# Kernel optimization log

Measured on AMD Instinct MI355X. Metric: run time of the kernel, lower is better.

## Reference

```python
import jax, jax.numpy as jnp
import numpy as np

HID = 1024
PRED_LEN = 96


def lstm_cell(x, h, c, Wih, Whh, bih, bhh):
    # PyTorch LSTMCell: gates ordered i, f, g, o
    gates = x @ Wih.T + h @ Whh.T + bih + bhh
    i, f, g, o = jnp.split(gates, 4, axis=-1)
    c_new = jax.nn.sigmoid(f) * c + jax.nn.sigmoid(i) * jnp.tanh(g)
    h_new = jax.nn.sigmoid(o) * jnp.tanh(c_new)
    return h_new, c_new


def time_enc(idx, embs):
    # sum of 4 embedding lookups -> [..., time_encode_dim]
    return sum(e[idx[..., k]] for k, e in enumerate(embs))


def setup_inputs() -> dict:
    key = jax.random.key(0)
    ks = jax.random.split(key, 32)
    B, T, IN, OUT, H, TE = 256, 128, 7, 7, HID, 3
    d = {}
    d["x"] = jax.random.normal(ks[0], (B, T, IN), jnp.float32)
    d["y"] = jax.random.normal(ks[1], (B, PRED_LEN, OUT), jnp.float32)
    d["x_time_encode"] = jax.random.randint(ks[2], (B, T, 4), 0, 7)
    d["y_time_encode"] = jax.random.randint(ks[3], (B, PRED_LEN, 4), 0, 7)
    sizes = (12, 31, 24, 7)
    for i, n in enumerate(sizes):
        d[f"emb{i}"] = jax.random.normal(ks[4 + i], (n, TE), jnp.float32)
    ins = (IN + TE, H, H)
    s = float(1.0 / np.sqrt(H))
    for l in range(3):
        d[f"Wih{l}"] = jax.random.uniform(ks[8 + 4 * l], (4 * H, ins[l]), jnp.float32, -s, s)
        d[f"Whh{l}"] = jax.random.uniform(ks[9 + 4 * l], (4 * H, H), jnp.float32, -s, s)
        d[f"bih{l}"] = jax.random.uniform(ks[10 + 4 * l], (4 * H,), jnp.float32, -s, s)
        d[f"bhh{l}"] = jax.random.uniform(ks[11 + 4 * l], (4 * H,), jnp.float32, -s, s)
    d["fcW"] = jax.random.uniform(ks[20], (OUT, H), jnp.float32, -s, s)
    d["fcb"] = jax.random.uniform(ks[21], (OUT,), jnp.float32, -s, s)
    return d


def reference(x, y, x_time_encode, y_time_encode, emb0, emb1, emb2, emb3,
              Wih0, Whh0, bih0, bhh0, Wih1, Whh1, bih1, bhh1,
              Wih2, Whh2, bih2, bhh2, fcW, fcb):
    embs = (emb0, emb1, emb2, emb3)
    layers = ((Wih0, Whh0, bih0, bhh0),
              (Wih1, Whh1, bih1, bhh1),
              (Wih2, Whh2, bih2, bhh2))
    B = x.shape[0]
    H = Whh0.shape[1]

    # encode: concat time embedding, run stacked LSTM over time (dropout_rate=0 -> no-op)
    xin = jnp.concatenate([x, time_enc(x_time_encode, embs)], axis=-1)  # [B,T,in+te]
    h0 = tuple(jnp.zeros((B, H), x.dtype) for _ in range(3))

    def run_layers(hs, cs, inp):
        nh, nc = [], []
        for l, (Wih, Whh, bih, bhh) in enumerate(layers):
            h, c = lstm_cell(inp, hs[l], cs[l], Wih, Whh, bih, bhh)
            nh.append(h)
            nc.append(c)
            inp = h
        return tuple(nh), tuple(nc)

    def enc_step(carry, xt):
        hs, cs = carry
        hs, cs = run_layers(hs, cs, xt)
        return (hs, cs), None

    (hs, cs), _ = jax.lax.scan(enc_step, (h0, h0), xin.swapaxes(0, 1))

    y0 = hs[-1] @ fcW.T + fcb  # [B, out]

    def dec_step(carry, te_idx):
        hs, cs, y_prev = carry
        inp = jnp.concatenate([y_prev, time_enc(te_idx, embs)], axis=-1)
        hs, cs = run_layers(hs, cs, inp)
        yt = hs[-1] @ fcW.T + fcb
        return (hs, cs, yt), yt

    _, ys = jax.lax.scan(dec_step, (hs, cs, y0),
                         y_time_encode[:, :PRED_LEN - 1].swapaxes(0, 1))
    # [B, predict_len, out]
    return jnp.concatenate([y0[:, None], ys.swapaxes(0, 1)], axis=1)
```

## Files before the change

kernel.cpp:

```cpp
#include <hip/hip_runtime.h>

#define HID   1024
#define BATCH 256
#define TSEQ  128
#define PRED  96
#define IND   7
#define OUTD  7
#define SK    10

typedef __attribute__((ext_vector_type(8))) _Float16 f16x8;
typedef __attribute__((ext_vector_type(4))) float    f32x4;

#define BM   64
#define BN   64
#define GSTR 68

__device__ __forceinline__ float sigmoidf_fast(float x) {
  return 1.0f / (1.0f + __expf(-x));
}
__device__ __forceinline__ float tanhf_fast(float x) {
  float ax = fabsf(x);
  float e  = __expf(-2.0f * ax);
  float r  = (1.0f - e) / (1.0f + e);
  return copysignf(r, x);
}

template<int AUX>
__device__ __forceinline__ void async_cp16(const void* g, void* l) {
  __builtin_amdgcn_global_load_lds(
      (const __attribute__((address_space(1))) void*)g,
      (__attribute__((address_space(3))) void*)l, 16, 0, AUX);
}

#define WBAR(N) asm volatile("s_waitcnt vmcnt(" #N ")\n\ts_barrier" ::: "memory")
#define BARO()  asm volatile("s_barrier" ::: "memory")

__global__ __launch_bounds__(256) void prep_kernel(
    const float* __restrict__ Wih0, const float* __restrict__ Whh0,
    const float* __restrict__ bih0, const float* __restrict__ bhh0,
    const float* __restrict__ Wih1, const float* __restrict__ Whh1,
    const float* __restrict__ bih1, const float* __restrict__ bhh1,
    const float* __restrict__ Wih2, const float* __restrict__ Whh2,
    const float* __restrict__ bih2, const float* __restrict__ bhh2,
    _Float16* __restrict__ B0, _Float16* __restrict__ B1, _Float16* __restrict__ B2,
    float* __restrict__ W0p, float* __restrict__ biasP)
{
  size_t e = (size_t)blockIdx.x * 256 + threadIdx.x;
  const size_t S0 = (size_t)4096 * 1024;
  const size_t S1 = (size_t)4096 * 2048;
  if (e < S0) {
    int n = (int)(e >> 10), k = (int)(e & 1023);
    int nb = n >> 6, gate = (n >> 4) & 3, u = n & 15;
    int r = gate * 1024 + nb * 16 + u;
    B0[e] = (_Float16)Whh0[(size_t)r * 1024 + k];
  } else if (e < S0 + S1) {
    size_t q = e - S0;
    int n = (int)(q >> 11), k = (int)(q & 2047);
    int nb = n >> 6, gate = (n >> 4) & 3, u = n & 15;
    int r = gate * 1024 + nb * 16 + u;
    float v = (k < 1024) ? Wih1[(size_t)r * 1024 + k]
                         : Whh1[(size_t)r * 1024 + (k - 1024)];
    B1[q] = (_Float16)v;
  } else if (e < S0 + 2 * S1) {
    size_t q = e - S0 - S1;
    int n = (int)(q >> 11), k = (int)(q & 2047);
    int nb = n >> 6, gate = (n >> 4) & 3, u = n & 15;
    int r = gate * 1024 + nb * 16 + u;
    float v = (k < 1024) ? Wih2[(size_t)r * 1024 + k]
                         : Whh2[(size_t)r * 1024 + (k - 1024)];
    B2[q] = (_Float16)v;
  } else if (e < S0 + 2 * S1 + 40960) {
    int q = (int)(e - S0 - 2 * S1);
    int n = q / 10, k = q - n * 10;
    int nb = n >> 6, gate = (n >> 4) & 3, u = n & 15;
    int r = gate * 1024 + nb * 16 + u;
    W0p[q] = Wih0[(size_t)r * 10 + k];
  } else if (e < S0 + 2 * S1 + 40960 + 12288) {
    int q = (int)(e - S0 - 2 * S1 - 40960);
    int l = q >> 12, n = q & 4095;
    int nb = n >> 6, gate = (n >> 4) & 3, u = n & 15;
    int r = gate * 1024 + nb * 16 + u;
    const float* bi = (l == 0) ? bih0 : (l == 1) ? bih1 : bih2;
    const float* bh = (l == 0) ? bhh0 : (l == 1) ? bhh1 : bhh2;
    biasP[q] = bi[r] + bh[r];
  }
}

__global__ __launch_bounds__(256) void lstm_wave(
    int d,
    _Float16* __restrict__ h0p0, _Float16* __restrict__ h0p1,
    _Float16* __restrict__ h1p0, _Float16* __restrict__ h1p1,
    _Float16* __restrict__ h2p0, _Float16* __restrict__ h2p1,
    const _Float16* __restrict__ B0g, const _Float16* __restrict__ B1g,
    const _Float16* __restrict__ B2g,
    const float* __restrict__ biasP, const float* __restrict__ W0p,
    float* __restrict__ c0, float* __restrict__ c1, float* __restrict__ c2,
    const float* __restrict__ x, const int* __restrict__ xte,
    const float* __restrict__ e0, const float* __restrict__ e1,
    const float* __restrict__ e2, const float* __restrict__ e3)
{
  __shared__ __align__(16) char smem[32768];
  __shared__ float SmallIn[BM * SK];
  __shared__ float W0s[BN * 11];

  const int layer = blockIdx.y >> 2;
  const int mb = blockIdx.y & 3, nb = blockIdx.x;
  const int t = d - layer;
  if (t < 0 || t >= TSEQ) return;
  const int p = d & 1;

  const _Float16 *A1, *A2; _Float16* ho; const _Float16* Bm;
  const float* bias; float* cst; int Kdim;
  if (layer == 0) {
    A1 = p ? h0p1 : h0p0; A2 = A1;              ho = p ? h0p0 : h0p1;
    Bm = B0g; bias = biasP;        cst = c0; Kdim = 1024;
  } else if (layer == 1) {
    A1 = p ? h0p1 : h0p0; A2 = p ? h1p1 : h1p0; ho = p ? h1p0 : h1p1;
    Bm = B1g; bias = biasP + 4096; cst = c1; Kdim = 2048;
  } else {
    A1 = p ? h1p1 : h1p0; A2 = p ? h2p1 : h2p0; ho = p ? h2p0 : h2p1;
    Bm = B2g; bias = biasP + 8192; cst = c2; Kdim = 2048;
  }
  const int Mbase = mb * BM;
  const int tid = threadIdx.x;

  if (layer == 0 && tid < BM) {
    int Mg = Mbase + tid;
    float v[SK];
    const float* xp = x + ((size_t)Mg * TSEQ + t) * IND;
#pragma unroll
    for (int i = 0; i < IND; ++i) v[i] = xp[i];
    const int* ip = xte + ((size_t)Mg * TSEQ + t) * 4;
    int i0 = ip[0], i1 = ip[1], i2 = ip[2], i3 = ip[3];
#pragma unroll
    for (int dd = 0; dd < 3; ++dd)
      v[IND + dd] = e0[i0 * 3 + dd] + e1[i1 * 3 + dd] + e2[i2 * 3 + dd] + e3[i3 * 3 + dd];
#pragma unroll
    for (int i = 0; i < SK; ++i) SmallIn[tid * SK + i] = v[i];
    const float* wp = W0p + (size_t)(nb * BN + tid) * SK;
#pragma unroll
    for (int i = 0; i < SK; ++i) W0s[tid * 11 + i] = wp[i];
  }

  _Float16* As = (_Float16*)smem;
  _Float16* Bs = (_Float16*)(smem + 16384);

  const int w = tid >> 6, lane = tid & 63;
  const int quad = lane >> 4, l16 = lane & 15;
  const int dr = lane >> 4, ds = lane & 15;

  size_t a_goff[4], b_goff[4];
  int lds_off[4];
#pragma unroll
  for (int i = 0; i < 4; ++i) {
    int lrow = w * 16 + i * 4 + dr;
    int sg = ds ^ (i * 4 + dr);
    a_goff[i] = (size_t)(Mbase + lrow) * (HID * 2) + (size_t)sg * 16;
    b_goff[i] = (size_t)(nb * BN + lrow) * ((size_t)Kdim * 2) + (size_t)sg * 16;
    lds_off[i] = lrow * 256 + ds * 16;
  }

  f32x4 acc[4] = {};

  for (int kk = 0; kk < Kdim; kk += 128) {
    const char* Abase = (kk < 1024)
        ? ((const char*)A1 + (size_t)kk * 2)
        : ((const char*)A2 + (size_t)(kk - 1024) * 2);
    const char* Bbase = (const char*)Bm + (size_t)kk * 2;
#pragma unroll
    for (int i = 0; i < 4; ++i) {
      async_cp16<0>(Abase + a_goff[i], smem + lds_off[i]);
      async_cp16<0>(Bbase + b_goff[i], smem + 16384 + lds_off[i]);
    }
    __syncthreads();
#pragma unroll
    for (int ks = 0; ks < 4; ++ks) {
      int segq = (ks * 4 + quad) ^ l16;
      f16x8 bf = *reinterpret_cast<const f16x8*>(Bs + (w * 16 + l16) * 128 + segq * 8);
#pragma unroll
      for (int mt = 0; mt < 4; ++mt) {
        f16x8 af = *reinterpret_cast<const f16x8*>(As + (mt * 16 + l16) * 128 + segq * 8);
        acc[mt] = __builtin_amdgcn_mfma_f32_16x16x32_f16(af, bf, acc[mt], 0, 0, 0);
      }
    }
    __syncthreads();
  }

  float* Gs = (float*)smem;
#pragma unroll
  for (int mt = 0; mt < 4; ++mt) {
    int row = mt * 16 + quad * 4;
    int col = w * 16 + l16;
#pragma unroll
    for (int r = 0; r < 4; ++r)
      Gs[(row + r) * GSTR + col] = acc[mt][r];
  }
  __syncthreads();

#pragma unroll
  for (int i = 0; i < 4; ++i) {
    int m = (tid >> 4) + i * 16;
    int u = tid & 15;
    float gi = Gs[m * GSTR + u];
    float gf = Gs[m * GSTR + 16 + u];
    float gg = Gs[m * GSTR + 32 + u];
    float go = Gs[m * GSTR + 48 + u];
    int nbase = nb * BN;
    gi += bias[nbase + u];
    gf += bias[nbase + 16 + u];
    gg += bias[nbase + 32 + u];
    go += bias[nbase + 48 + u];
    if (layer == 0) {
#pragma unroll
      for (int k = 0; k < SK; ++k) {
        float sv = SmallIn[m * SK + k];
        gi += sv * W0s[u * 11 + k];
        gf += sv * W0s[(16 + u) * 11 + k];
        gg += sv * W0s[(32 + u) * 11 + k];
        go += sv * W0s[(48 + u) * 11 + k];
      }
    }
    size_t cidx = (size_t)(Mbase + m) * HID + (size_t)nb * 16 + u;
    float cold = cst[cidx];
    float cn = sigmoidf_fast(gf) * cold + sigmoidf_fast(gi) * tanhf_fast(gg);
    float hn = sigmoidf_fast(go) * tanhf_fast(cn);
    cst[cidx] = cn;
    ho[cidx] = (_Float16)hn;
  }
}

template<int KC, int MODE>
__global__ __launch_bounds__(256, 2) void dec_phase(
    const _Float16* __restrict__ A1g, const _Float16* __restrict__ A2g,
    _Float16* __restrict__ ho, const _Float16* __restrict__ Bm,
    const float* __restrict__ biasL, const float* __restrict__ W0p,
    float* __restrict__ cst, float* __restrict__ out,
    const int* __restrict__ yte,
    const float* __restrict__ e0, const float* __restrict__ e1,
    const float* __restrict__ e2, const float* __restrict__ e3,
    const float* __restrict__ fcW, const float* __restrict__ fcb, int s)
{
  __shared__ __align__(16) char smem[2 * 24576];
  __shared__ float Gs[32 * GSTR];
  __shared__ float SmallIn[32 * SK];
  __shared__ float W0s[64 * 11];

  const int tid = threadIdx.x;
  const int nb = blockIdx.x, mb = blockIdx.y;
  const int Mbase = mb * 32;

  if (MODE == 1) {
    if (tid < 32) {
      int Mg = Mbase + tid;
      float v[SK];
      const float* yp = out + (size_t)Mg * (PRED * OUTD) + s * OUTD;
#pragma unroll
      for (int i = 0; i < OUTD; ++i) v[i] = yp[i];
      const int* ip = yte + ((size_t)Mg * PRED + s) * 4;
      int i0 = ip[0], i1 = ip[1], i2 = ip[2], i3 = ip[3];
#pragma unroll
      for (int dd = 0; dd < 3; ++dd)
        v[IND + dd] = e0[i0 * 3 + dd] + e1[i1 * 3 + dd]
                    + e2[i2 * 3 + dd] + e3[i3 * 3 + dd];
#pragma unroll
      for (int i = 0; i < SK; ++i) SmallIn[tid * SK + i] = v[i];
    }
    if (tid < 64) {
      const float* wp = W0p + (size_t)(nb * 64 + tid) * SK;
#pragma unroll
      for (int i = 0; i < SK; ++i) W0s[tid * 11 + i] = wp[i];
    }
  }

  const int w = tid >> 6, lane = tid & 63;
  const int quad = lane >> 4, l16 = lane & 15;

  int a_src[2], a_dst[2], b_src[4], b_dst[4];
#pragma unroll
  for (int op = 0; op < 2; ++op) {
    int j = op * 256 + tid, row = j >> 4, seg = j & 15;
    a_src[op] = (Mbase + row) * 2048 + ((seg ^ (row & 15)) * 16);
    a_dst[op] = row * 256 + seg * 16;
  }
#pragma unroll
  for (int op = 0; op < 4; ++op) {
    int j = op * 256 + tid, row = j >> 4, seg = j & 15;
    b_src[op] = (nb * 64 + row) * (KC * 256) + ((seg ^ (row & 15)) * 16);
    b_dst[op] = 8192 + row * 256 + seg * 16;
  }

#define PISSUE(c) do { \
    const char* Ab_ = (KC == 8 || (c) < 8) \
        ? ((const char*)A1g + (size_t)(c) * 256) \
        : ((const char*)A2g + (size_t)((c) - 8) * 256); \
    const char* Bb_ = (const char*)Bm + (size_t)(c) * 256; \
    char* L_ = smem + ((c) & 1) * 24576; \
    _Pragma("unroll") \
    for (int i_ = 0; i_ < 2; ++i_) async_cp16<0>(Ab_ + a_src[i_], L_ + a_dst[i_]); \
    _Pragma("unroll") \
    for (int i_ = 0; i_ < 4; ++i_) async_cp16<0>(Bb_ + b_src[i_], L_ + b_dst[i_]); \
  } while (0)

  f32x4 acc[2] = {};
  PISSUE(0);
#pragma unroll
  for (int c = 0; c < KC; ++c) {
    if (c + 1 < KC) { PISSUE(c + 1); WBAR(6); }
    else            { WBAR(0); }
    const _Float16* As = (const _Float16*)(smem + (c & 1) * 24576);
    const _Float16* Bs = As + 4096;
#pragma unroll
    for (int ks = 0; ks < 4; ++ks) {
      int sq = (ks * 4 + quad) ^ l16;
      f16x8 bf = *reinterpret_cast<const f16x8*>(Bs + (w * 16 + l16) * 128 + sq * 8);
#pragma unroll
      for (int mt = 0; mt < 2; ++mt) {
        f16x8 af = *reinterpret_cast<const f16x8*>(As + (mt * 16 + l16) * 128 + sq * 8);
        acc[mt] = __builtin_amdgcn_mfma_f32_16x16x32_f16(af, bf, acc[mt], 0, 0, 0);
      }
    }
    BARO();
  }
#undef PISSUE

#pragma unroll
  for (int mt = 0; mt < 2; ++mt) {
    int row = mt * 16 + quad * 4;
    int col = w * 16 + l16;
#pragma unroll
    for (int r = 0; r < 4; ++r)
      Gs[(row + r) * GSTR + col] = acc[mt][r];
  }
  __syncthreads();

  const int u = tid & 15;
#pragma unroll
  for (int i = 0; i < 2; ++i) {
    int m = (tid >> 4) + i * 16;
    int nbase = nb * 64;
    float gi = Gs[m * GSTR + u]      + biasL[nbase + u];
    float gf = Gs[m * GSTR + 16 + u] + biasL[nbase + 16 + u];
    float gg = Gs[m * GSTR + 32 + u] + biasL[nbase + 32 + u];
    float go = Gs[m * GSTR + 48 + u] + biasL[nbase + 48 + u];
    if (MODE == 1) {
#pragma unroll
      for (int k = 0; k < SK; ++k) {
        float sv = SmallIn[m * SK + k];
        gi += sv * W0s[u * 11 + k];
        gf += sv * W0s[(16 + u) * 11 + k];
        gg += sv * W0s[(32 + u) * 11 + k];
        go += sv * W0s[(48 + u) * 11 + k];
      }
    }
    size_t cidx = (size_t)(Mbase + m) * HID + (size_t)nb * 16 + u;
    float cold = cst[cidx];
    float cn = sigmoidf_fast(gf) * cold + sigmoidf_fast(gi) * tanhf_fast(gg);
    float hn = sigmoidf_fast(go) * tanhf_fast(cn);
    cst[cidx] = cn;
    ho[cidx] = (_Float16)hn;
    if (MODE == 3) {
#pragma unroll
      for (int o = 0; o < OUTD; ++o) {
        float r = hn * fcW[(size_t)o * HID + nb * 16 + u];
        r += __shfl_xor(r, 1, 16);
        r += __shfl_xor(r, 2, 16);
        r += __shfl_xor(r, 4, 16);
        r += __shfl_xor(r, 8, 16);
        if (u == 0)
          atomicAdd(&out[(size_t)(Mbase + m) * (PRED * OUTD) + (s + 1) * OUTD + o],
                    r + ((nb == 0) ? fcb[o] : 0.0f));
      }
    }
  }
}

__global__ __launch_bounds__(256) void fc_kernel(
    const _Float16* __restrict__ h2, const float* __restrict__ fcW,
    const float* __restrict__ fcb, float* __restrict__ out)
{
  int wv = threadIdx.x >> 6, lane = threadIdx.x & 63;
  int row = blockIdx.x * 4 + wv;
  const _Float16* hp = h2 + (size_t)row * HID + lane * 16;
  float hv[16];
#pragma unroll
  for (int i = 0; i < 16; ++i) hv[i] = (float)hp[i];
  float acc[OUTD];
#pragma unroll
  for (int o = 0; o < OUTD; ++o) {
    const float* wp = fcW + (size_t)o * HID + lane * 16;
    float a = 0.f;
#pragma unroll
    for (int i = 0; i < 16; ++i) a += hv[i] * wp[i];
    acc[o] = a;
  }
#pragma unroll
  for (int o = 0; o < OUTD; ++o)
#pragma unroll
    for (int off = 32; off >= 1; off >>= 1)
      acc[o] += __shfl_xor(acc[o], off, 64);
  if (lane == 0) {
#pragma unroll
    for (int o = 0; o < OUTD; ++o)
      out[(size_t)row * (PRED * OUTD) + o] = acc[o] + fcb[o];
  }
}

extern "C" void kernel_launch(void* const* d_in, const int* in_sizes, int n_in,
                              void* d_out, int out_size, void* d_ws, size_t ws_size,
                              hipStream_t stream) {
  const float* x   = (const float*)d_in[0];
  const int*   xte = (const int*)d_in[2];
  const int*   yte = (const int*)d_in[3];
  const float* e0  = (const float*)d_in[4];
  const float* e1  = (const float*)d_in[5];
  const float* e2  = (const float*)d_in[6];
  const float* e3  = (const float*)d_in[7];
  const float* Wih0 = (const float*)d_in[8];
  const float* Whh0 = (const float*)d_in[9];
  const float* bih0 = (const float*)d_in[10];
  const float* bhh0 = (const float*)d_in[11];
  const float* Wih1 = (const float*)d_in[12];
  const float* Whh1 = (const float*)d_in[13];
  const float* bih1 = (const float*)d_in[14];
  const float* bhh1 = (const float*)d_in[15];
  const float* Wih2 = (const float*)d_in[16];
  const float* Whh2 = (const float*)d_in[17];
  const float* bih2 = (const float*)d_in[18];
  const float* bhh2 = (const float*)d_in[19];
  const float* fcW = (const float*)d_in[20];
  const float* fcb = (const float*)d_in[21];
  float* out = (float*)d_out;

  char* ws = (char*)d_ws;
  _Float16* B0   = (_Float16*)(ws);
  _Float16* B1   = (_Float16*)(ws + 8388608);
  _Float16* B2   = (_Float16*)(ws + 25165824);
  float*    W0p  = (float*)(ws + 41943040);
  float*    biasP= (float*)(ws + 42106880);
  char*     hp0  = ws + 42156032;
  float*    cbuf = (float*)(ws + 43728896);
  char*     hp1  = ws + 46874624;

  hipMemsetAsync(out, 0, (size_t)out_size * 4, stream);
  hipMemsetAsync(hp0, 0, 4718592, stream);
  hipMemsetAsync(hp1, 0, 1572864, stream);

  prep_kernel<<<82128, 256, 0, stream>>>(Wih0, Whh0, bih0, bhh0,
                                         Wih1, Whh1, bih1, bhh1,
                                         Wih2, Whh2, bih2, bhh2,
                                         B0, B1, B2, W0p, biasP);

  auto hb = [&](int l, int par) -> _Float16* {
    return (_Float16*)((par ? hp1 : hp0) + (size_t)l * 524288);
  };
  float* cl[3] = {cbuf, cbuf + 262144, cbuf + 524288};

  for (int d = 0; d < TSEQ + 2; ++d) {
    lstm_wave<<<dim3(64, 12), 256, 0, stream>>>(
        d, hb(0,0), hb(0,1), hb(1,0), hb(1,1), hb(2,0), hb(2,1),
        B0, B1, B2, biasP, W0p, cl[0], cl[1], cl[2],
        x, xte, e0, e1, e2, e3);
  }

  fc_kernel<<<64, 256, 0, stream>>>(hb(2,0), fcW, fcb, out);

  int p0 = 0, p1 = 1, p2 = 0;
  const dim3 dgrid(64, 8);
  for (int s = 0; s < PRED - 1; ++s) {
    dec_phase<8, 1><<<dgrid, 256, 0, stream>>>(
        hb(0, p0), hb(0, p0), hb(0, 1 - p0), B0,
        biasP, W0p, cl[0], out, yte, e0, e1, e2, e3, fcW, fcb, s);
    dec_phase<16, 2><<<dgrid, 256, 0, stream>>>(
        hb(0, 1 - p0), hb(1, p1), hb(1, 1 - p1), B1,
        biasP + 4096, W0p, cl[1], out, yte, e0, e1, e2, e3, fcW, fcb, s);
    dec_phase<16, 3><<<dgrid, 256, 0, stream>>>(
        hb(1, 1 - p1), hb(2, p2), hb(2, 1 - p2), B2,
        biasP + 8192, W0p, cl[2], out, yte, e0, e1, e2, e3, fcW, fcb, s);
    p0 ^= 1; p1 ^= 1; p2 ^= 1;
  }
}
```

Baseline: 7.808 ms.

## Split decoder recurrent GEMMs and overlap them with dependent layer phases

The decoder now splits each layer's gate GEMM into its recurrent part (h_prev of the same layer times Whh) and its input part. The recurrent part is precomputed into global partial-gate buffers by otherwise idle blocks in the previous phase, so each launch runs two independent tasks side by side and the critical path per phase shrinks to K=1024. Tiles grow to 64 rows of M, which halves the number of M blocks per task, and h buffers are updated in place instead of ping-ponged. The cost is extra global traffic for fp32 partial gates and more complex phase ordering, and in-place h updates rely on the recurrent GEMM reading h before the pointwise step overwrites it.

```diff
diff --git a/kernel.cpp b/kernel.cpp
--- a/kernel.cpp
+++ b/kernel.cpp
@@ -229,102 +229,64 @@
   }
 }
 
-template<int KC, int MODE>
-__global__ __launch_bounds__(256, 2) void dec_phase(
-    const _Float16* __restrict__ A1g, const _Float16* __restrict__ A2g,
-    _Float16* __restrict__ ho, const _Float16* __restrict__ Bm,
-    const float* __restrict__ biasL, const float* __restrict__ W0p,
-    float* __restrict__ cst, float* __restrict__ out,
-    const int* __restrict__ yte,
-    const float* __restrict__ e0, const float* __restrict__ e1,
-    const float* __restrict__ e2, const float* __restrict__ e3,
-    const float* __restrict__ fcW, const float* __restrict__ fcb, int s)
+__device__ __forceinline__ void gemm_k1024(
+    const char* Ab, const char* Bb, size_t bstr,
+    char* smem, f32x4 (&acc)[4], int Mbase, int nb, int tid)
 {
-  __shared__ __align__(16) char smem[2 * 24576];
-  __shared__ float Gs[32 * GSTR];
-  __shared__ float SmallIn[32 * SK];
-  __shared__ float W0s[64 * 11];
-
-  const int tid = threadIdx.x;
-  const int nb = blockIdx.x, mb = blockIdx.y;
-  const int Mbase = mb * 32;
-
-  if (MODE == 1) {
-    if (tid < 32) {
-      int Mg = Mbase + tid;
-      float v[SK];
-      const float* yp = out + (size_t)Mg * (PRED * OUTD) + s * OUTD;
-#pragma unroll
-      for (int i = 0; i < OUTD; ++i) v[i] = yp[i];
-      const int* ip = yte + ((size_t)Mg * PRED + s) * 4;
-      int i0 = ip[0], i1 = ip[1], i2 = ip[2], i3 = ip[3];
-#pragma unroll
-      for (int dd = 0; dd < 3; ++dd)
-        v[IND + dd] = e0[i0 * 3 + dd] + e1[i1 * 3 + dd]
-                    + e2[i2 * 3 + dd] + e3[i3 * 3 + dd];
-#pragma unroll
-      for (int i = 0; i < SK; ++i) SmallIn[tid * SK + i] = v[i];
-    }
-    if (tid < 64) {
-      const float* wp = W0p + (size_t)(nb * 64 + tid) * SK;
-#pragma unroll
-      for (int i = 0; i < SK; ++i) W0s[tid * 11 + i] = wp[i];
-    }
-  }
-
   const int w = tid >> 6, lane = tid & 63;
   const int quad = lane >> 4, l16 = lane & 15;
-
-  int a_src[2], a_dst[2], b_src[4], b_dst[4];
-#pragma unroll
-  for (int op = 0; op < 2; ++op) {
-    int j = op * 256 + tid, row = j >> 4, seg = j & 15;
-    a_src[op] = (Mbase + row) * 2048 + ((seg ^ (row & 15)) * 16);
-    a_dst[op] = row * 256 + seg * 16;
-  }
-#pragma unroll
-  for (int op = 0; op < 4; ++op) {
-    int j = op * 256 + tid, row = j >> 4, seg = j & 15;
-    b_src[op] = (nb * 64 + row) * (KC * 256) + ((seg ^ (row & 15)) * 16);
-    b_dst[op] = 8192 + row * 256 + seg * 16;
-  }
-
-#define PISSUE(c) do { \
-    const char* Ab_ = (KC == 8 || (c) < 8) \
-        ? ((const char*)A1g + (size_t)(c) * 256) \
-        : ((const char*)A2g + (size_t)((c) - 8) * 256); \
-    const char* Bb_ = (const char*)Bm + (size_t)(c) * 256; \
-    char* L_ = smem + ((c) & 1) * 24576; \
+  size_t a_src[4], b_src[4];
+  int ldst[4];
+#pragma unroll
+  for (int i = 0; i < 4; ++i) {
+    int lrow = w * 16 + i * 4 + quad;
+    int sg = l16 ^ (i * 4 + quad);
+    a_src[i] = (size_t)(Mbase + lrow) * 2048 + (size_t)sg * 16;
+    b_src[i] = (size_t)(nb * 64 + lrow) * bstr + (size_t)sg * 16;
+    ldst[i] = lrow * 256 + l16 * 16;
+  }
+#define GISSUE(c) do { \
+    char* L_ = smem + ((c) & 1) * 32768; \
+    const char* Ab_ = Ab + (size_t)(c) * 256; \
+    const char* Bb_ = Bb + (size_t)(c) * 256; \
     _Pragma("unroll") \
-    for (int i_ = 0; i_ < 2; ++i_) async_cp16<0>(Ab_ + a_src[i_], L_ + a_dst[i_]); \
-    _Pragma("unroll") \
-    for (int i_ = 0; i_ < 4; ++i_) async_cp16<0>(Bb_ + b_src[i_], L_ + b_dst[i_]); \
-  } while (0)
-
-  f32x4 acc[2] = {};
-  PISSUE(0);
-#pragma unroll
-  for (int c = 0; c < KC; ++c) {
-    if (c + 1 < KC) { PISSUE(c + 1); WBAR(6); }
-    else            { WBAR(0); }
-    const _Float16* As = (const _Float16*)(smem + (c & 1) * 24576);
-    const _Float16* Bs = As + 4096;
+    for (int i_ = 0; i_ < 4; ++i_) { \
+      async_cp16<0>(Ab_ + a_src[i_], L_ + ldst[i_]); \
+      async_cp16<0>(Bb_ + b_src[i_], L_ + 16384 + ldst[i_]); \
+    } } while (0)
+  GISSUE(0);
+#pragma unroll
+  for (int c = 0; c < 8; ++c) {
+    if (c + 1 < 8) { GISSUE(c + 1); WBAR(8); }
+    else           { WBAR(0); }
+    const _Float16* As = (const _Float16*)(smem + (c & 1) * 32768);
+    const _Float16* Bs = As + 8192;
 #pragma unroll
     for (int ks = 0; ks < 4; ++ks) {
       int sq = (ks * 4 + quad) ^ l16;
       f16x8 bf = *reinterpret_cast<const f16x8*>(Bs + (w * 16 + l16) * 128 + sq * 8);
 #pragma unroll
-      for (int mt = 0; mt < 2; ++mt) {
+      for (int mt = 0; mt < 4; ++mt) {
         f16x8 af = *reinterpret_cast<const f16x8*>(As + (mt * 16 + l16) * 128 + sq * 8);
         acc[mt] = __builtin_amdgcn_mfma_f32_16x16x32_f16(af, bf, acc[mt], 0, 0, 0);
       }
     }
     BARO();
   }
-#undef PISSUE
-
-#pragma unroll
-  for (int mt = 0; mt < 2; ++mt) {
+#undef GISSUE
+}
+
+template<int MODE>
+__device__ __forceinline__ void pointwise(
+    f32x4 (&acc)[4], float* Gs, const float* SmallIn, const float* W0s,
+    const float* biasL, float* cst, _Float16* ho,
+    float* out, const float* fcW, const float* fcb,
+    int s, int Mbase, int nb, int tid)
+{
+  const int w = tid >> 6, lane = tid & 63;
+  const int quad = lane >> 4, l16 = lane & 15;
+#pragma unroll
+  for (int mt = 0; mt < 4; ++mt) {
     int row = mt * 16 + quad * 4;
     int col = w * 16 + l16;
 #pragma unroll
@@ -332,10 +294,9 @@
       Gs[(row + r) * GSTR + col] = acc[mt][r];
   }
   __syncthreads();
-
   const int u = tid & 15;
 #pragma unroll
-  for (int i = 0; i < 2; ++i) {
+  for (int i = 0; i < 4; ++i) {
     int m = (tid >> 4) + i * 16;
     int nbase = nb * 64;
     float gi = Gs[m * GSTR + u]      + biasL[nbase + u];
@@ -358,7 +319,7 @@
     float hn = sigmoidf_fast(go) * tanhf_fast(cn);
     cst[cidx] = cn;
     ho[cidx] = (_Float16)hn;
-    if (MODE == 3) {
+    if (MODE == 2) {
 #pragma unroll
       for (int o = 0; o < OUTD; ++o) {
         float r = hn * fcW[(size_t)o * HID + nb * 16 + u];
@@ -371,6 +332,109 @@
                     r + ((nb == 0) ? fcb[o] : 0.0f));
       }
     }
+  }
+}
+
+template<int PH>
+__global__ __launch_bounds__(256, 2) void dec_duo(
+    _Float16* __restrict__ h0, _Float16* __restrict__ h1, _Float16* __restrict__ h2,
+    const _Float16* __restrict__ B0g, const _Float16* __restrict__ B1g,
+    const _Float16* __restrict__ B2g,
+    const float* __restrict__ biasP, const float* __restrict__ W0p,
+    float* __restrict__ c0, float* __restrict__ c1, float* __restrict__ c2,
+    float* __restrict__ out, const int* __restrict__ yte,
+    const float* __restrict__ e0, const float* __restrict__ e1,
+    const float* __restrict__ e2, const float* __restrict__ e3,
+    const float* __restrict__ fcW, const float* __restrict__ fcb,
+    float* __restrict__ gp0, float* __restrict__ gp1, float* __restrict__ gp2,
+    int s)
+{
+  __shared__ __align__(16) char smem[65536];
+  __shared__ float SmallIn[64 * SK];
+  __shared__ float W0s[64 * 11];
+
+  const int tid = threadIdx.x;
+  const int nb = blockIdx.x;
+  const int task = (PH == 3) ? 1 : ((int)blockIdx.y >> 2);
+  const int mb   = (PH == 3) ? (int)blockIdx.y : ((int)blockIdx.y & 3);
+  const int Mbase = mb * 64;
+  float* Gs = (float*)smem;
+  f32x4 acc[4] = {};
+
+  const size_t bidx = ((size_t)(mb * 64 + nb) * 256 + tid) * 16;
+
+  if (PH == 0) {
+    if (task == 0) {
+      if (tid < 64) {
+        int Mg = Mbase + tid;
+        float v[SK];
+        const float* yp = out + (size_t)Mg * (PRED * OUTD) + s * OUTD;
+#pragma unroll
+        for (int i = 0; i < OUTD; ++i) v[i] = yp[i];
+        const int* ip = yte + ((size_t)Mg * PRED + s) * 4;
+        int i0 = ip[0], i1 = ip[1], i2 = ip[2], i3 = ip[3];
+#pragma unroll
+        for (int dd = 0; dd < 3; ++dd)
+          v[IND + dd] = e0[i0 * 3 + dd] + e1[i1 * 3 + dd]
+                      + e2[i2 * 3 + dd] + e3[i3 * 3 + dd];
+#pragma unroll
+        for (int i = 0; i < SK; ++i) SmallIn[tid * SK + i] = v[i];
+        const float* wp = W0p + (size_t)(nb * 64 + tid) * SK;
+#pragma unroll
+        for (int i = 0; i < SK; ++i) W0s[tid * 11 + i] = wp[i];
+      }
+#pragma unroll
+      for (int mt = 0; mt < 4; ++mt)
+        acc[mt] = *reinterpret_cast<const f32x4*>(gp0 + bidx + mt * 4);
+      __syncthreads();
+      pointwise<1>(acc, Gs, SmallIn, W0s, biasP, c0, h0,
+                   out, fcW, fcb, s, Mbase, nb, tid);
+    } else {
+      gemm_k1024((const char*)h1, (const char*)B1g + 2048, 4096,
+                 smem, acc, Mbase, nb, tid);
+#pragma unroll
+      for (int mt = 0; mt < 4; ++mt)
+        *reinterpret_cast<f32x4*>(gp1 + bidx + mt * 4) = acc[mt];
+    }
+  } else if (PH == 1) {
+    if (task == 0) {
+#pragma unroll
+      for (int mt = 0; mt < 4; ++mt)
+        acc[mt] = *reinterpret_cast<const f32x4*>(gp1 + bidx + mt * 4);
+      gemm_k1024((const char*)h0, (const char*)B1g, 4096,
+                 smem, acc, Mbase, nb, tid);
+      pointwise<0>(acc, Gs, SmallIn, W0s, biasP + 4096, c1, h1,
+                   out, fcW, fcb, s, Mbase, nb, tid);
+    } else {
+      gemm_k1024((const char*)h2, (const char*)B2g + 2048, 4096,
+                 smem, acc, Mbase, nb, tid);
+#pragma unroll
+      for (int mt = 0; mt < 4; ++mt)
+        *reinterpret_cast<f32x4*>(gp2 + bidx + mt * 4) = acc[mt];
+    }
+  } else if (PH == 2) {
+    if (task == 0) {
+#pragma unroll
+      for (int mt = 0; mt < 4; ++mt)
+        acc[mt] = *reinterpret_cast<const f32x4*>(gp2 + bidx + mt * 4);
+      gemm_k1024((const char*)h1, (const char*)B2g, 4096,
+                 smem, acc, Mbase, nb, tid);
+      pointwise<2>(acc, Gs, SmallIn, W0s, biasP + 8192, c2, h2,
+                   out, fcW, fcb, s, Mbase, nb, tid);
+    } else {
+      if (s >= PRED - 2) return;
+      gemm_k1024((const char*)h0, (const char*)B0g, 2048,
+                 smem, acc, Mbase, nb, tid);
+#pragma unroll
+      for (int mt = 0; mt < 4; ++mt)
+        *reinterpret_cast<f32x4*>(gp0 + bidx + mt * 4) = acc[mt];
+    }
+  } else {
+    gemm_k1024((const char*)h0, (const char*)B0g, 2048,
+               smem, acc, Mbase, nb, tid);
+#pragma unroll
+    for (int mt = 0; mt < 4; ++mt)
+      *reinterpret_cast<f32x4*>(gp0 + bidx + mt * 4) = acc[mt];
   }
 }
 
@@ -440,6 +504,9 @@
   char*     hp0  = ws + 42156032;
   float*    cbuf = (float*)(ws + 43728896);
   char*     hp1  = ws + 46874624;
+  float*    gp0  = (float*)(ws + 48447488);
+  float*    gp1  = (float*)(ws + 52641792);
+  float*    gp2  = (float*)(ws + 56836096);
 
   hipMemsetAsync(out, 0, (size_t)out_size * 4, stream);
   hipMemsetAsync(hp0, 0, 4718592, stream);
@@ -462,20 +529,25 @@
         x, xte, e0, e1, e2, e3);
   }
 
-  fc_kernel<<<64, 256, 0, stream>>>(hb(2,0), fcW, fcb, out);
-
-  int p0 = 0, p1 = 1, p2 = 0;
-  const dim3 dgrid(64, 8);
+  _Float16* h0 = hb(0, 0);
+  _Float16* h1 = hb(1, 1);
+  _Float16* h2 = hb(2, 0);
+
+  fc_kernel<<<64, 256, 0, stream>>>(h2, fcW, fcb, out);
+
+  dec_duo<3><<<dim3(64, 4), 256, 0, stream>>>(
+      h0, h1, h2, B0, B1, B2, biasP, W0p, cl[0], cl[1], cl[2],
+      out, yte, e0, e1, e2, e3, fcW, fcb, gp0, gp1, gp2, 0);
+
   for (int s = 0; s < PRED - 1; ++s) {
-    dec_phase<8, 1><<<dgrid, 256, 0, stream>>>(
-        hb(0, p0), hb(0, p0), hb(0, 1 - p0), B0,
-        biasP, W0p, cl[0], out, yte, e0, e1, e2, e3, fcW, fcb, s);
-    dec_phase<16, 2><<<dgrid, 256, 0, stream>>>(
-        hb(0, 1 - p0), hb(1, p1), hb(1, 1 - p1), B1,
-        biasP + 4096, W0p, cl[1], out, yte, e0, e1, e2, e3, fcW, fcb, s);
-    dec_phase<16, 3><<<dgrid, 256, 0, stream>>>(
-        hb(1, 1 - p1), hb(2, p2), hb(2, 1 - p2), B2,
-        biasP + 8192, W0p, cl[2], out, yte, e0, e1, e2, e3, fcW, fcb, s);
-    p0 ^= 1; p1 ^= 1; p2 ^= 1;
-  }
-}
+    dec_duo<0><<<dim3(64, 8), 256, 0, stream>>>(
+        h0, h1, h2, B0, B1, B2, biasP, W0p, cl[0], cl[1], cl[2],
+        out, yte, e0, e1, e2, e3, fcW, fcb, gp0, gp1, gp2, s);
+    dec_duo<1><<<dim3(64, 8), 256, 0, stream>>>(
+        h0, h1, h2, B0, B1, B2, biasP, W0p, cl[0], cl[1], cl[2],
+        out, yte, e0, e1, e2, e3, fcW, fcb, gp0, gp1, gp2, s);
+    dec_duo<2><<<dim3(64, 8), 256, 0, stream>>>(
+        h0, h1, h2, B0, B1, B2, biasP, W0p, cl[0], cl[1], cl[2],
+        out, yte, e0, e1, e2, e3, fcW, fcb, gp0, gp1, gp2, s);
+  }
+}
```

Result: slower. 8.229 ms (+5.4%).

## Enlarge decoder tiles to 64 rows and deepen async copy pipeline to 4 stages

Applied to the files above, without the earlier changes.

The decoder phase kernel now processes 64 batch rows per block instead of 32 and launches half as many blocks. Each B weight tile is therefore reused across more rows, which lowers weight traffic from global memory. The shared-memory ring grows from 2 to 4 stages with 3 chunks prefetched, and the copy index mapping is rewritten. In exchange there are fewer blocks (256) and the larger LDS footprint limits occupancy to one block per CU, so latency hiding rests on the deeper prefetch.

```diff
diff --git a/kernel.cpp b/kernel.cpp
--- a/kernel.cpp
+++ b/kernel.cpp
@@ -230,7 +230,7 @@
 }
 
 template<int KC, int MODE>
-__global__ __launch_bounds__(256, 2) void dec_phase(
+__global__ __launch_bounds__(256, 1) void dec_phase(
     const _Float16* __restrict__ A1g, const _Float16* __restrict__ A2g,
     _Float16* __restrict__ ho, const _Float16* __restrict__ Bm,
     const float* __restrict__ biasL, const float* __restrict__ W0p,
@@ -240,53 +240,46 @@
     const float* __restrict__ e2, const float* __restrict__ e3,
     const float* __restrict__ fcW, const float* __restrict__ fcb, int s)
 {
-  __shared__ __align__(16) char smem[2 * 24576];
-  __shared__ float Gs[32 * GSTR];
-  __shared__ float SmallIn[32 * SK];
-  __shared__ float W0s[64 * 11];
+  __shared__ __align__(16) char smem[4 * 32768];
+  __shared__ float Gs[BM * GSTR];
+  __shared__ float SmallIn[BM * SK];
+  __shared__ float W0s[BN * 11];
 
   const int tid = threadIdx.x;
   const int nb = blockIdx.x, mb = blockIdx.y;
-  const int Mbase = mb * 32;
-
-  if (MODE == 1) {
-    if (tid < 32) {
-      int Mg = Mbase + tid;
-      float v[SK];
-      const float* yp = out + (size_t)Mg * (PRED * OUTD) + s * OUTD;
-#pragma unroll
-      for (int i = 0; i < OUTD; ++i) v[i] = yp[i];
-      const int* ip = yte + ((size_t)Mg * PRED + s) * 4;
-      int i0 = ip[0], i1 = ip[1], i2 = ip[2], i3 = ip[3];
-#pragma unroll
-      for (int dd = 0; dd < 3; ++dd)
-        v[IND + dd] = e0[i0 * 3 + dd] + e1[i1 * 3 + dd]
-                    + e2[i2 * 3 + dd] + e3[i3 * 3 + dd];
-#pragma unroll
-      for (int i = 0; i < SK; ++i) SmallIn[tid * SK + i] = v[i];
-    }
-    if (tid < 64) {
-      const float* wp = W0p + (size_t)(nb * 64 + tid) * SK;
-#pragma unroll
-      for (int i = 0; i < SK; ++i) W0s[tid * 11 + i] = wp[i];
-    }
+  const int Mbase = mb * BM;
+
+  if (MODE == 1 && tid < BM) {
+    int Mg = Mbase + tid;
+    float v[SK];
+    const float* yp = out + (size_t)Mg * (PRED * OUTD) + s * OUTD;
+#pragma unroll
+    for (int i = 0; i < OUTD; ++i) v[i] = yp[i];
+    const int* ip = yte + ((size_t)Mg * PRED + s) * 4;
+    int i0 = ip[0], i1 = ip[1], i2 = ip[2], i3 = ip[3];
+#pragma unroll
+    for (int dd = 0; dd < 3; ++dd)
+      v[IND + dd] = e0[i0 * 3 + dd] + e1[i1 * 3 + dd]
+                  + e2[i2 * 3 + dd] + e3[i3 * 3 + dd];
+#pragma unroll
+    for (int i = 0; i < SK; ++i) SmallIn[tid * SK + i] = v[i];
+    const float* wp = W0p + (size_t)(nb * BN + tid) * SK;
+#pragma unroll
+    for (int i = 0; i < SK; ++i) W0s[tid * 11 + i] = wp[i];
   }
 
   const int w = tid >> 6, lane = tid & 63;
   const int quad = lane >> 4, l16 = lane & 15;
 
-  int a_src[2], a_dst[2], b_src[4], b_dst[4];
-#pragma unroll
-  for (int op = 0; op < 2; ++op) {
-    int j = op * 256 + tid, row = j >> 4, seg = j & 15;
-    a_src[op] = (Mbase + row) * 2048 + ((seg ^ (row & 15)) * 16);
-    a_dst[op] = row * 256 + seg * 16;
-  }
-#pragma unroll
-  for (int op = 0; op < 4; ++op) {
-    int j = op * 256 + tid, row = j >> 4, seg = j & 15;
-    b_src[op] = (nb * 64 + row) * (KC * 256) + ((seg ^ (row & 15)) * 16);
-    b_dst[op] = 8192 + row * 256 + seg * 16;
+  size_t a_goff[4], b_goff[4];
+  int lds_off[4];
+#pragma unroll
+  for (int i = 0; i < 4; ++i) {
+    int lrow = w * 16 + i * 4 + quad;
+    int sg = l16 ^ (i * 4 + quad);
+    a_goff[i] = (size_t)(Mbase + lrow) * 2048 + (size_t)sg * 16;
+    b_goff[i] = (size_t)(nb * BN + lrow) * ((size_t)KC * 256) + (size_t)sg * 16;
+    lds_off[i] = lrow * 256 + l16 * 16;
   }
 
 #define PISSUE(c) do { \
@@ -294,27 +287,31 @@
         ? ((const char*)A1g + (size_t)(c) * 256) \
         : ((const char*)A2g + (size_t)((c) - 8) * 256); \
     const char* Bb_ = (const char*)Bm + (size_t)(c) * 256; \
-    char* L_ = smem + ((c) & 1) * 24576; \
+    char* L_ = smem + ((c) & 3) * 32768; \
     _Pragma("unroll") \
-    for (int i_ = 0; i_ < 2; ++i_) async_cp16<0>(Ab_ + a_src[i_], L_ + a_dst[i_]); \
-    _Pragma("unroll") \
-    for (int i_ = 0; i_ < 4; ++i_) async_cp16<0>(Bb_ + b_src[i_], L_ + b_dst[i_]); \
-  } while (0)
-
-  f32x4 acc[2] = {};
+    for (int i_ = 0; i_ < 4; ++i_) { \
+      async_cp16<0>(Ab_ + a_goff[i_], L_ + lds_off[i_]); \
+      async_cp16<0>(Bb_ + b_goff[i_], L_ + 16384 + lds_off[i_]); \
+    } } while (0)
+
+  f32x4 acc[4] = {};
   PISSUE(0);
+  PISSUE(1);
+  PISSUE(2);
 #pragma unroll
   for (int c = 0; c < KC; ++c) {
-    if (c + 1 < KC) { PISSUE(c + 1); WBAR(6); }
-    else            { WBAR(0); }
-    const _Float16* As = (const _Float16*)(smem + (c & 1) * 24576);
-    const _Float16* Bs = As + 4096;
+    if (c + 3 < KC)       { PISSUE(c + 3); WBAR(24); }
+    else if (c + 3 == KC) { WBAR(16); }
+    else if (c + 2 == KC) { WBAR(8); }
+    else                  { WBAR(0); }
+    const _Float16* As = (const _Float16*)(smem + (c & 3) * 32768);
+    const _Float16* Bs = As + 8192;
 #pragma unroll
     for (int ks = 0; ks < 4; ++ks) {
       int sq = (ks * 4 + quad) ^ l16;
       f16x8 bf = *reinterpret_cast<const f16x8*>(Bs + (w * 16 + l16) * 128 + sq * 8);
 #pragma unroll
-      for (int mt = 0; mt < 2; ++mt) {
+      for (int mt = 0; mt < 4; ++mt) {
         f16x8 af = *reinterpret_cast<const f16x8*>(As + (mt * 16 + l16) * 128 + sq * 8);
         acc[mt] = __builtin_amdgcn_mfma_f32_16x16x32_f16(af, bf, acc[mt], 0, 0, 0);
       }
@@ -324,7 +321,7 @@
 #undef PISSUE
 
 #pragma unroll
-  for (int mt = 0; mt < 2; ++mt) {
+  for (int mt = 0; mt < 4; ++mt) {
     int row = mt * 16 + quad * 4;
     int col = w * 16 + l16;
 #pragma unroll
@@ -335,9 +332,9 @@
 
   const int u = tid & 15;
 #pragma unroll
-  for (int i = 0; i < 2; ++i) {
+  for (int i = 0; i < 4; ++i) {
     int m = (tid >> 4) + i * 16;
-    int nbase = nb * 64;
+    int nbase = nb * BN;
     float gi = Gs[m * GSTR + u]      + biasL[nbase + u];
     float gf = Gs[m * GSTR + 16 + u] + biasL[nbase + 16 + u];
     float gg = Gs[m * GSTR + 32 + u] + biasL[nbase + 32 + u];
@@ -465,7 +462,7 @@
   fc_kernel<<<64, 256, 0, stream>>>(hb(2,0), fcW, fcb, out);
 
   int p0 = 0, p1 = 1, p2 = 0;
-  const dim3 dgrid(64, 8);
+  const dim3 dgrid(64, 4);
   for (int s = 0; s < PRED - 1; ++s) {
     dec_phase<8, 1><<<dgrid, 256, 0, stream>>>(
         hb(0, p0), hb(0, p0), hb(0, 1 - p0), B0,
```

Measured after the change: 8.688 ms. 11.3% more time.

## Enlarge decoder GEMM tiles to 64x64 with 512 threads and 256-wide K chunks

Applied to the files above, without the earlier changes.

Retiles the decode-phase kernel from 32-row by 64-col blocks with 128-wide K chunks to 64-row blocks with 256-wide K chunks, using 8 waves per block and half as many blocks. Fewer, larger K iterations reduce barrier and async-copy issue overhead, and each B weight tile is now reused across twice as many rows. The cost is 128KB of double-buffered LDS per block, with the gate scratch aliased onto that buffer. Only 256 blocks are launched, which lowers parallelism on a GPU with many CUs and leaves one block per CU.

```diff
diff --git a/kernel.cpp b/kernel.cpp
--- a/kernel.cpp
+++ b/kernel.cpp
@@ -230,7 +230,7 @@
 }
 
 template<int KC, int MODE>
-__global__ __launch_bounds__(256, 2) void dec_phase(
+__global__ __launch_bounds__(512, 2) void dec_phase(
     const _Float16* __restrict__ A1g, const _Float16* __restrict__ A2g,
     _Float16* __restrict__ ho, const _Float16* __restrict__ Bm,
     const float* __restrict__ biasL, const float* __restrict__ W0p,
@@ -240,17 +240,17 @@
     const float* __restrict__ e2, const float* __restrict__ e3,
     const float* __restrict__ fcW, const float* __restrict__ fcb, int s)
 {
-  __shared__ __align__(16) char smem[2 * 24576];
-  __shared__ float Gs[32 * GSTR];
-  __shared__ float SmallIn[32 * SK];
+  __shared__ __align__(16) char smem[2 * 65536];
+  __shared__ float SmallIn[64 * SK];
   __shared__ float W0s[64 * 11];
+  float* Gs = (float*)smem;
 
   const int tid = threadIdx.x;
   const int nb = blockIdx.x, mb = blockIdx.y;
-  const int Mbase = mb * 32;
+  const int Mbase = mb * 64;
 
   if (MODE == 1) {
-    if (tid < 32) {
+    if (tid < 64) {
       int Mg = Mbase + tid;
       float v[SK];
       const float* yp = out + (size_t)Mg * (PRED * OUTD) + s * OUTD;
@@ -264,8 +264,6 @@
                     + e2[i2 * 3 + dd] + e3[i3 * 3 + dd];
 #pragma unroll
       for (int i = 0; i < SK; ++i) SmallIn[tid * SK + i] = v[i];
-    }
-    if (tid < 64) {
       const float* wp = W0p + (size_t)(nb * 64 + tid) * SK;
 #pragma unroll
       for (int i = 0; i < SK; ++i) W0s[tid * 11 + i] = wp[i];
@@ -274,50 +272,46 @@
 
   const int w = tid >> 6, lane = tid & 63;
   const int quad = lane >> 4, l16 = lane & 15;
-
-  int a_src[2], a_dst[2], b_src[4], b_dst[4];
-#pragma unroll
-  for (int op = 0; op < 2; ++op) {
-    int j = op * 256 + tid, row = j >> 4, seg = j & 15;
-    a_src[op] = (Mbase + row) * 2048 + ((seg ^ (row & 15)) * 16);
-    a_dst[op] = row * 256 + seg * 16;
-  }
+  const int rowh = w >> 2, colw = w & 3;
+
+  int a_src[4], b_src[4];
 #pragma unroll
   for (int op = 0; op < 4; ++op) {
-    int j = op * 256 + tid, row = j >> 4, seg = j & 15;
-    b_src[op] = (nb * 64 + row) * (KC * 256) + ((seg ^ (row & 15)) * 16);
-    b_dst[op] = 8192 + row * 256 + seg * 16;
-  }
+    int j = op * 512 + tid, row = j >> 5, seg = j & 31;
+    int sw = (seg ^ (row & 15)) * 16;
+    a_src[op] = (Mbase + row) * 2048 + sw;
+    b_src[op] = (nb * 64 + row) * (KC * 512) + sw;
+  }
+  const int dstb = tid * 16;
 
 #define PISSUE(c) do { \
-    const char* Ab_ = (KC == 8 || (c) < 8) \
-        ? ((const char*)A1g + (size_t)(c) * 256) \
-        : ((const char*)A2g + (size_t)((c) - 8) * 256); \
-    const char* Bb_ = (const char*)Bm + (size_t)(c) * 256; \
-    char* L_ = smem + ((c) & 1) * 24576; \
+    const char* Ab_ = (KC == 4 || (c) < 4) \
+        ? ((const char*)A1g + (size_t)(c) * 512) \
+        : ((const char*)A2g + (size_t)((c) - 4) * 512); \
+    const char* Bb_ = (const char*)Bm + (size_t)(c) * 512; \
+    char* L_ = smem + ((c) & 1) * 65536; \
     _Pragma("unroll") \
-    for (int i_ = 0; i_ < 2; ++i_) async_cp16<0>(Ab_ + a_src[i_], L_ + a_dst[i_]); \
-    _Pragma("unroll") \
-    for (int i_ = 0; i_ < 4; ++i_) async_cp16<0>(Bb_ + b_src[i_], L_ + b_dst[i_]); \
-  } while (0)
+    for (int i_ = 0; i_ < 4; ++i_) { \
+      async_cp16<0>(Ab_ + a_src[i_], L_ + i_ * 8192 + dstb); \
+      async_cp16<0>(Bb_ + b_src[i_], L_ + 32768 + i_ * 8192 + dstb); \
+    } } while (0)
 
   f32x4 acc[2] = {};
   PISSUE(0);
 #pragma unroll
   for (int c = 0; c < KC; ++c) {
-    if (c + 1 < KC) { PISSUE(c + 1); WBAR(6); }
+    if (c + 1 < KC) { PISSUE(c + 1); WBAR(8); }
     else            { WBAR(0); }
-    const _Float16* As = (const _Float16*)(smem + (c & 1) * 24576);
-    const _Float16* Bs = As + 4096;
-#pragma unroll
-    for (int ks = 0; ks < 4; ++ks) {
+    const _Float16* As = (const _Float16*)(smem + (c & 1) * 65536);
+    const _Float16* Bs = As + 16384;
+#pragma unroll
+    for (int ks = 0; ks < 8; ++ks) {
       int sq = (ks * 4 + quad) ^ l16;
-      f16x8 bf = *reinterpret_cast<const f16x8*>(Bs + (w * 16 + l16) * 128 + sq * 8);
-#pragma unroll
-      for (int mt = 0; mt < 2; ++mt) {
-        f16x8 af = *reinterpret_cast<const f16x8*>(As + (mt * 16 + l16) * 128 + sq * 8);
-        acc[mt] = __builtin_amdgcn_mfma_f32_16x16x32_f16(af, bf, acc[mt], 0, 0, 0);
-      }
+      f16x8 bf = *reinterpret_cast<const f16x8*>(Bs + (colw * 16 + l16) * 256 + sq * 8);
+      f16x8 a0 = *reinterpret_cast<const f16x8*>(As + (rowh * 32 + l16) * 256 + sq * 8);
+      f16x8 a1 = *reinterpret_cast<const f16x8*>(As + (rowh * 32 + 16 + l16) * 256 + sq * 8);
+      acc[0] = __builtin_amdgcn_mfma_f32_16x16x32_f16(a0, bf, acc[0], 0, 0, 0);
+      acc[1] = __builtin_amdgcn_mfma_f32_16x16x32_f16(a1, bf, acc[1], 0, 0, 0);
     }
     BARO();
   }
@@ -325,18 +319,18 @@
 
 #pragma unroll
   for (int mt = 0; mt < 2; ++mt) {
-    int row = mt * 16 + quad * 4;
-    int col = w * 16 + l16;
+    int row = rowh * 32 + mt * 16 + quad * 4;
+    int col = colw * 16 + l16;
 #pragma unroll
     for (int r = 0; r < 4; ++r)
       Gs[(row + r) * GSTR + col] = acc[mt][r];
   }
   __syncthreads();
 
-  const int u = tid & 15;
+  const int u = tid & 15, mr = tid >> 4;
 #pragma unroll
   for (int i = 0; i < 2; ++i) {
-    int m = (tid >> 4) + i * 16;
+    int m = mr + i * 32;
     int nbase = nb * 64;
     float gi = Gs[m * GSTR + u]      + biasL[nbase + u];
     float gf = Gs[m * GSTR + 16 + u] + biasL[nbase + 16 + u];
@@ -465,15 +459,15 @@
   fc_kernel<<<64, 256, 0, stream>>>(hb(2,0), fcW, fcb, out);
 
   int p0 = 0, p1 = 1, p2 = 0;
-  const dim3 dgrid(64, 8);
+  const dim3 dgrid(64, 4);
   for (int s = 0; s < PRED - 1; ++s) {
-    dec_phase<8, 1><<<dgrid, 256, 0, stream>>>(
+    dec_phase<4, 1><<<dgrid, 512, 0, stream>>>(
         hb(0, p0), hb(0, p0), hb(0, 1 - p0), B0,
         biasP, W0p, cl[0], out, yte, e0, e1, e2, e3, fcW, fcb, s);
-    dec_phase<16, 2><<<dgrid, 256, 0, stream>>>(
+    dec_phase<8, 2><<<dgrid, 512, 0, stream>>>(
         hb(0, 1 - p0), hb(1, p1), hb(1, 1 - p1), B1,
         biasP + 4096, W0p, cl[1], out, yte, e0, e1, e2, e3, fcW, fcb, s);
-    dec_phase<16, 3><<<dgrid, 256, 0, stream>>>(
+    dec_phase<8, 3><<<dgrid, 512, 0, stream>>>(
         hb(1, 1 - p1), hb(2, p2), hb(2, 1 - p2), B2,
         biasP + 8192, W0p, cl[2], out, yte, e0, e1, e2, e3, fcW, fcb, s);
     p0 ^= 1; p1 ^= 1; p2 ^= 1;
```

After: 7.528 ms. -3.6%, faster.
